# Kernel optimization log

Hardware: AMD Instinct MI355X
Metric: run time of the kernel (lower is better)

## Reference

```python
import jax, jax.numpy as jnp
import numpy as np

N_HEADS = 16
ROPE_BASE = 10000.0

def apply_rope(x):
    # x: [B, H, S, D] with D even; interleaved-pair RoPE (torchtune style)
    B, H, S, D = x.shape
    half = D // 2
    inv_freq = 1.0 / (ROPE_BASE ** (jnp.arange(0, half, dtype=jnp.float32) / half))
    angles = jnp.arange(S, dtype=jnp.float32)[:, None] * inv_freq[None, :]  # [S, D/2]
    cos = jnp.cos(angles)[None, None]  # [1,1,S,D/2]
    sin = jnp.sin(angles)[None, None]
    x1 = x[..., 0::2]
    x2 = x[..., 1::2]
    r1 = x1 * cos - x2 * sin
    r2 = x1 * sin + x2 * cos
    return jnp.stack([r1, r2], axis=-1).reshape(B, H, S, D)

def setup_inputs() -> dict:
    key = jax.random.key(0)
    ks = jax.random.split(key, 5)
    B, S, E = 2, 2048, 1024
    d_attn = 1024
    scale = 1.0 / np.sqrt(E)
    x = jax.random.normal(ks[0], (B, S, E), dtype=jnp.float32)
    Wq = jax.random.normal(ks[1], (d_attn, E), dtype=jnp.float32) * scale
    Wk = jax.random.normal(ks[2], (d_attn, E), dtype=jnp.float32) * scale
    Wv = jax.random.normal(ks[3], (d_attn, E), dtype=jnp.float32) * scale
    Wo = jax.random.normal(ks[4], (E, d_attn), dtype=jnp.float32) * scale
    return {"x": x, "Wq": Wq, "Wk": Wk, "Wv": Wv, "Wo": Wo}

def reference(x, Wq, Wk, Wv, Wo):
    B, S, E = x.shape
    d_attn = Wq.shape[0]
    hd = d_attn // N_HEADS
    attn_scale = 1.0 / np.sqrt(d_attn)
    # projections (nn.Linear: x @ W.T), split heads -> [B, H, S, hd]
    q = (x @ Wq.T).reshape(B, S, N_HEADS, hd).transpose(0, 2, 1, 3)
    k = (x @ Wk.T).reshape(B, S, N_HEADS, hd).transpose(0, 2, 1, 3)
    v = (x @ Wv.T).reshape(B, S, N_HEADS, hd).transpose(0, 2, 1, 3)
    q = apply_rope(q)
    k = apply_rope(k)
    scores = jnp.einsum('bhqd,bhkd->bhqk', q, k) * attn_scale  # [B,H,S,S]
    causal = jnp.tril(jnp.ones((S, S), dtype=bool))
    scores = jnp.where(causal[None, None], scores, -jnp.inf)
    probs = jax.nn.softmax(scores, axis=-1)  # dropout is identity in eval
    out = jnp.einsum('bhqk,bhkd->bhqd', probs, v)
    out = out.transpose(0, 2, 1, 3).reshape(B, S, d_attn)
    return out @ Wo.T
```

## Files before the change

kernel.cpp:

```cpp
#include <hip/hip_runtime.h>


typedef float  f32x4  __attribute__((ext_vector_type(4)));
typedef short  short8 __attribute__((ext_vector_type(8)));

#define MFMA16(a,b,c) __builtin_amdgcn_mfma_f32_16x16x32_bf16((a),(b),(c),0,0,0)
#define GLD_LDS16(g, l)                                                        \
  __builtin_amdgcn_global_load_lds(                                            \
      (const __attribute__((address_space(1))) unsigned int*)(g),              \
      (__attribute__((address_space(3))) unsigned int*)(l), 16, 0, 0)

__device__ __forceinline__ unsigned short f2bf(float f) {
  unsigned int x = __float_as_uint(f);
  x += 0x7fffu + ((x >> 16) & 1u);
  return (unsigned short)(x >> 16);
}
__device__ __forceinline__ float bf2f(unsigned short u) {
  return __uint_as_float(((unsigned int)u) << 16);
}

__global__ __launch_bounds__(256) void cvt_all(const float* __restrict__ x,
                                               const float* __restrict__ wq,
                                               const float* __restrict__ wk,
                                               const float* __restrict__ wv,
                                               const float* __restrict__ wo,
                                               ushort* __restrict__ dst) {
  const int i = blockIdx.x * 256 + threadIdx.x;
  const float* src;
  int off;
  if (i < 1048576) { src = x; off = i; }
  else {
    const int j = i - 1048576;
    const int wsel = j >> 18;
    off = j & 262143;
    src = (wsel == 0) ? wq : (wsel == 1) ? wk : (wsel == 2) ? wv : wo;
  }
  const float4 v = ((const float4*)src)[off];
  ushort4 o = make_ushort4(f2bf(v.x), f2bf(v.y), f2bf(v.z), f2bf(v.w));
  ((ushort4*)dst)[i] = o;
}

template<int MODE, int BN>
__global__ __launch_bounds__(256) void gemm_bt(const ushort* __restrict__ A,
                                               const ushort* __restrict__ B,
                                               void* __restrict__ Cv,
                                               int K) {
  constexpr int NI = BN / 32;
  __shared__ __align__(16) short As[128 * 32];
  __shared__ __align__(16) short Bs[BN * 32];
  const int tid  = threadIdx.x;
  const int lane = tid & 63, w = tid >> 6;
  const int ln   = lane & 15, quad = lane >> 4;
  const int wm   = w >> 1, wn = w & 1;
  const int m0 = blockIdx.y * 128, n0 = blockIdx.x * BN;

  const int srow = lane >> 2;
  const int schk = (lane & 3) * 8;
  const ushort* Ag0 = A + (size_t)(m0 + w * 32      + srow) * K + schk;
  const ushort* Ag1 = A + (size_t)(m0 + w * 32 + 16 + srow) * K + schk;
  const int brow = (BN == 128) ? w * 32 : w * 16;
  const ushort* Bg0 = B + (size_t)(n0 + brow + srow) * K + schk;
  const ushort* Bg1 = B + (size_t)(n0 + brow + 16 + srow) * K + schk;
  short* lA0 = As + (w * 32) * 32;
  short* lA1 = As + (w * 32 + 16) * 32;
  short* lB0 = Bs + brow * 32;
  short* lB1 = Bs + (brow + 16) * 32;

  int aoff[4], boff[NI];
#pragma unroll
  for (int i = 0; i < 4; i++)
    aoff[i] = (wm * 64 + i * 16 + ln) * 32 + quad * 8;
#pragma unroll
  for (int i = 0; i < NI; i++)
    boff[i] = (wn * (BN / 2) + i * 16 + ln) * 32 + quad * 8;
  f32x4 acc[4][NI] = {};

  for (int kt = 0; kt < K; kt += 32) {
    __syncthreads();
    GLD_LDS16(Ag0 + kt, lA0);
    GLD_LDS16(Ag1 + kt, lA1);
    GLD_LDS16(Bg0 + kt, lB0);
    if (BN == 128) GLD_LDS16(Bg1 + kt, lB1);
    __syncthreads();
    short8 av[4], bv[NI];
#pragma unroll
    for (int i = 0; i < 4; i++) av[i] = *(const short8*)&As[aoff[i]];
#pragma unroll
    for (int i = 0; i < NI; i++) bv[i] = *(const short8*)&Bs[boff[i]];
#pragma unroll
    for (int mi = 0; mi < 4; mi++)
#pragma unroll
      for (int ni = 0; ni < NI; ni++)
        acc[mi][ni] = MFMA16(av[mi], bv[ni], acc[mi][ni]);
  }

  if (MODE == 0) {
    ushort* Cq = (ushort*)Cv;
    if (n0 < 2048) {
      ushort* dst = Cq + (n0 < 1024 ? 0 : 4194304);
      const int nbase = (n0 < 1024) ? n0 : n0 - 1024;
#pragma unroll
      for (int mi = 0; mi < 4; mi++) {
        const int row = m0 + wm * 64 + mi * 16 + quad * 4;
#pragma unroll
        for (int ni = 0; ni < NI; ni++) {
          const int col = nbase + wn * (BN / 2) + ni * 16 + ln;
#pragma unroll
          for (int r = 0; r < 4; r++)
            dst[(size_t)(row + r) * 1024 + col] = f2bf(acc[mi][ni][r]);
        }
      }
    } else {
      ushort* vt = Cq + 8388608;
#pragma unroll
      for (int mi = 0; mi < 4; mi++) {
        const int sm = m0 + wm * 64 + mi * 16 + quad * 4;
        const int b = sm >> 11, s = sm & 2047;
#pragma unroll
        for (int ni = 0; ni < NI; ni++) {
          const int nv = (n0 - 2048) + wn * (BN / 2) + ni * 16 + ln;
          const int bh = b * 16 + (nv >> 6), d = nv & 63;
          ushort4 u = make_ushort4(f2bf(acc[mi][ni][0]), f2bf(acc[mi][ni][1]),
                                   f2bf(acc[mi][ni][2]), f2bf(acc[mi][ni][3]));
          *(ushort4*)&vt[((size_t)bh * 64 + d) * 2048 + s] = u;
        }
      }
    }
  } else {
    float* C = (float*)Cv;
#pragma unroll
    for (int mi = 0; mi < 4; mi++) {
      const int row = m0 + wm * 64 + mi * 16 + quad * 4;
#pragma unroll
      for (int ni = 0; ni < NI; ni++) {
        const int col = n0 + wn * (BN / 2) + ni * 16 + ln;
#pragma unroll
        for (int r = 0; r < 4; r++)
          C[(size_t)(row + r) * 1024 + col] = acc[mi][ni][r];
      }
    }
  }
}

__global__ __launch_bounds__(256) void ropek(ushort* __restrict__ qk) {
  const int g  = blockIdx.x * 256 + threadIdx.x;
  const int P0 = g << 2;
  const int mv = P0 >> 9;
  const int s  = mv & 2047;
  const int i0 = P0 & 31;
  const float scale = (mv < 4096) ? 0.04508422002778011f : 1.0f;
  const float sf = (float)s;
  short8 u = *(short8*)&qk[(size_t)P0 * 2];
  short8 ov;
#pragma unroll
  for (int t = 0; t < 4; t++) {
    const float invf = __builtin_amdgcn_exp2f(-(float)(i0 + t) * 0.4152410118579865f);
    const float rev  = sf * invf * 0.15915494309189535f;
    const float rr   = rev - floorf(rev);
    const float sn = __builtin_amdgcn_sinf(rr);
    const float cs = __builtin_amdgcn_cosf(rr);
    const float x1 = bf2f((unsigned short)u[2 * t]);
    const float x2 = bf2f((unsigned short)u[2 * t + 1]);
    ov[2 * t]     = (short)f2bf((x1 * cs - x2 * sn) * scale);
    ov[2 * t + 1] = (short)f2bf((x1 * sn + x2 * cs) * scale);
  }
  *(short8*)&qk[(size_t)P0 * 2] = ov;
}

__global__ __launch_bounds__(256) void attnk(const ushort* __restrict__ q,
                                             const ushort* __restrict__ k,
                                             const ushort* __restrict__ vt,
                                             ushort* __restrict__ Opart,
                                             float* __restrict__ Lpart) {
  __shared__ __align__(16) short Ks[64 * 72];
  __shared__ __align__(16) short Vs[64 * 72];
  __shared__ __align__(16) short Ps[4 * 16 * 72];
  const int tid  = threadIdx.x;
  const int lane = tid & 63, w = tid >> 6;
  const int ln   = lane & 15, quad = lane >> 4;
  const int x = blockIdx.x, bh = blockIdx.y, par = blockIdx.z;
  const int b = bh >> 4, h = bh & 15;
  const int jA = x, jB = 31 - x;
  short* Pw = Ps + w * 1152;

  const size_t qbA = ((size_t)(b * 2048 + jA * 64 + w * 16 + ln)) * 1024 + h * 64;
  const size_t qbB = ((size_t)(b * 2048 + jB * 64 + w * 16 + ln)) * 1024 + h * 64;
  const short8 aqA0 = *(const short8*)&q[qbA + quad * 8];
  const short8 aqA1 = *(const short8*)&q[qbA + 32 + quad * 8];
  const short8 aqB0 = *(const short8*)&q[qbB + quad * 8];
  const short8 aqB1 = *(const short8*)&q[qbB + 32 + quad * 8];

  f32x4 oA[4] = {}, oB[4] = {};
  float lsA[4] = {0.f, 0.f, 0.f, 0.f}, lsB[4] = {0.f, 0.f, 0.f, 0.f};

  const int s0 = tid, s1 = tid + 256;
  const int r0 = s0 >> 3, c0 = (s0 & 7) * 8;
  const int r1 = s1 >> 3, c1 = (s1 & 7) * 8;
  const ushort* kg0 = k  + ((size_t)(b * 2048 + r0)) * 1024 + h * 64 + c0;
  const ushort* kg1 = k  + ((size_t)(b * 2048 + r1)) * 1024 + h * 64 + c1;
  const ushort* vg0 = vt + ((size_t)(bh * 64 + r0)) * 2048 + c0;
  const ushort* vg1 = vt + ((size_t)(bh * 64 + r1)) * 2048 + c1;
  const int wK0 = r0 * 72 + c0, wK1 = r1 * 72 + c1;

  for (int t = par; t <= jB; t += 2) {
    __syncthreads();
    *(short8*)&Ks[wK0] = *(const short8*)(kg0 + (size_t)t * 65536);
    *(short8*)&Ks[wK1] = *(const short8*)(kg1 + (size_t)t * 65536);
    *(short8*)&Vs[wK0] = *(const short8*)(vg0 + t * 64);
    *(short8*)&Vs[wK1] = *(const short8*)(vg1 + t * 64);
    __syncthreads();

    const bool actA = (t <= jA);
    f32x4 scA[4], scB[4];
#pragma unroll
    for (int ct = 0; ct < 4; ct++) {
      const short8 bk0 = *(const short8*)&Ks[(ct * 16 + ln) * 72 + quad * 8];
      const short8 bk1 = *(const short8*)&Ks[(ct * 16 + ln) * 72 + 32 + quad * 8];
      f32x4 z = {0.f, 0.f, 0.f, 0.f};
      z = MFMA16(aqB0, bk0, z);
      z = MFMA16(aqB1, bk1, z);
      scB[ct] = z;
      if (actA) {
        f32x4 y = {0.f, 0.f, 0.f, 0.f};
        y = MFMA16(aqA0, bk0, y);
        y = MFMA16(aqA1, bk1, y);
        scA[ct] = y;
      }
    }
    if (t == jB) {
#pragma unroll
      for (int ct = 0; ct < 4; ct++) {
        const int kv = (t << 6) + ct * 16 + ln;
#pragma unroll
        for (int r = 0; r < 4; r++)
          if (kv > jB * 64 + w * 16 + quad * 4 + r) scB[ct][r] = -100000.0f;
      }
    }
    if (actA && t == jA) {
#pragma unroll
      for (int ct = 0; ct < 4; ct++) {
        const int kv = (t << 6) + ct * 16 + ln;
#pragma unroll
        for (int r = 0; r < 4; r++)
          if (kv > jA * 64 + w * 16 + quad * 4 + r) scA[ct][r] = -100000.0f;
      }
    }

    short8 bv0[4], bv1[4];
#pragma unroll
    for (int dt = 0; dt < 4; dt++) {
      bv0[dt] = *(const short8*)&Vs[(dt * 16 + ln) * 72 + quad * 8];
      bv1[dt] = *(const short8*)&Vs[(dt * 16 + ln) * 72 + 32 + quad * 8];
    }

#pragma unroll
    for (int ct = 0; ct < 4; ct++)
#pragma unroll
      for (int r = 0; r < 4; r++) {
        const float p = __builtin_amdgcn_exp2f(scB[ct][r]);
        lsB[r] += p;
        Pw[(quad * 4 + r) * 72 + ct * 16 + ln] = (short)f2bf(p);
      }
    {
      const short8 ap0 = *(const short8*)&Pw[ln * 72 + quad * 8];
      const short8 ap1 = *(const short8*)&Pw[ln * 72 + 32 + quad * 8];
#pragma unroll
      for (int dt = 0; dt < 4; dt++) {
        oB[dt] = MFMA16(ap0, bv0[dt], oB[dt]);
        oB[dt] = MFMA16(ap1, bv1[dt], oB[dt]);
      }
    }
    if (actA) {
#pragma unroll
      for (int ct = 0; ct < 4; ct++)
#pragma unroll
        for (int r = 0; r < 4; r++) {
          const float p = __builtin_amdgcn_exp2f(scA[ct][r]);
          lsA[r] += p;
          Pw[(quad * 4 + r) * 72 + ct * 16 + ln] = (short)f2bf(p);
        }
      const short8 ap0 = *(const short8*)&Pw[ln * 72 + quad * 8];
      const short8 ap1 = *(const short8*)&Pw[ln * 72 + 32 + quad * 8];
#pragma unroll
      for (int dt = 0; dt < 4; dt++) {
        oA[dt] = MFMA16(ap0, bv0[dt], oA[dt]);
        oA[dt] = MFMA16(ap1, bv1[dt], oA[dt]);
      }
    }
  }

#pragma unroll
  for (int off = 1; off < 16; off <<= 1)
#pragma unroll
    for (int r = 0; r < 4; r++) {
      lsA[r] += __shfl_xor(lsA[r], off, 64);
      lsB[r] += __shfl_xor(lsB[r], off, 64);
    }

  const size_t pidx = ((size_t)(x * 32 + bh)) * 2 + par;
  const size_t ob = pidx * 8192;
#pragma unroll
  for (int r = 0; r < 4; r++) {
    const int row = w * 16 + quad * 4 + r;
#pragma unroll
    for (int dt = 0; dt < 4; dt++) {
      Opart[ob + row * 64 + dt * 16 + ln]        = f2bf(oA[dt][r]);
      Opart[ob + 4096 + row * 64 + dt * 16 + ln] = f2bf(oB[dt][r]);
    }
    if (ln == 0) {
      Lpart[pidx * 128 + row]      = lsA[r];
      Lpart[pidx * 128 + 64 + row] = lsB[r];
    }
  }
}

__global__ __launch_bounds__(256) void mergek(const ushort* __restrict__ Opart,
                                              const float* __restrict__ Lpart,
                                              ushort* __restrict__ ctx) {
  const int x = blockIdx.x, bh = blockIdx.y, tau = blockIdx.z;
  const int b = bh >> 4, h = bh & 15;
  const int j = tau ? 31 - x : x;
  const int tid = threadIdx.x;
  const int row = tid >> 2, c0 = (tid & 3) * 16;
  const size_t p0 = ((size_t)(x * 32 + bh)) * 2;
  const size_t base0 = p0 * 8192 + (size_t)tau * 4096 + row * 64 + c0;
  const size_t base1 = base0 + 8192;
  const float l = Lpart[p0 * 128 + tau * 64 + row] +
                  Lpart[(p0 + 1) * 128 + tau * 64 + row];
  const float inv = 1.0f / l;
  const short8 u0a = *(const short8*)&Opart[base0];
  const short8 u0b = *(const short8*)&Opart[base0 + 8];
  const short8 u1a = *(const short8*)&Opart[base1];
  const short8 u1b = *(const short8*)&Opart[base1 + 8];
  short8 oa, ob;
#pragma unroll
  for (int i = 0; i < 8; i++) {
    oa[i] = (short)f2bf((bf2f((unsigned short)u0a[i]) +
                         bf2f((unsigned short)u1a[i])) * inv);
    ob[i] = (short)f2bf((bf2f((unsigned short)u0b[i]) +
                         bf2f((unsigned short)u1b[i])) * inv);
  }
  const size_t dst = ((size_t)(b * 2048 + j * 64 + row)) * 1024 + h * 64 + c0;
  *(short8*)&ctx[dst]     = oa;
  *(short8*)&ctx[dst + 8] = ob;
}

extern "C" void kernel_launch(void* const* d_in, const int* in_sizes, int n_in,
                              void* d_out, int out_size, void* d_ws, size_t ws_size,
                              hipStream_t stream) {
  const float* x  = (const float*)d_in[0];
  const float* Wq = (const float*)d_in[1];
  const float* Wk = (const float*)d_in[2];
  const float* Wv = (const float*)d_in[3];
  const float* Wo = (const float*)d_in[4];
  float* out = (float*)d_out;
  char* ws = (char*)d_ws;

  ushort* xb  = (ushort*)(ws);
  ushort* wqb = (ushort*)(ws + (size_t)(8  << 20));
  ushort* qb  = (ushort*)(ws + (size_t)(16 << 20));
  ushort* kb  = (ushort*)(ws + (size_t)(24 << 20));
  ushort* vtb = (ushort*)(ws + (size_t)(32 << 20));
  ushort* ctx = (ushort*)(ws + (size_t)(40 << 20));
  float*  lpart = (float*)(ws);
  ushort* opart = (ushort*)d_out;

  cvt_all<<<8192, 256, 0, stream>>>(x, Wq, Wk, Wv, Wo, xb);
  gemm_bt<0, 128><<<dim3(24, 32), 256, 0, stream>>>(xb, wqb, (void*)qb, 1024);
  ropek<<<4096, 256, 0, stream>>>(qb);
  attnk<<<dim3(16, 32, 2), 256, 0, stream>>>(qb, kb, vtb, opart, lpart);
  mergek<<<dim3(16, 32, 2), 256, 0, stream>>>(opart, lpart, ctx);
  gemm_bt<2, 64><<<dim3(16, 32), 256, 0, stream>>>(ctx, wqb + 3145728 , (void*)out, 1024);
}
```

Baseline: 206.2 us.

## Fuse RoPE into QKV GEMM epilogue and drop split-KV attention merge

```diff
diff --git a/kernel.cpp b/kernel.cpp
--- a/kernel.cpp
+++ b/kernel.cpp
@@ -99,6 +99,15 @@
     if (n0 < 2048) {
       ushort* dst = Cq + (n0 < 1024 ? 0 : 4194304);
       const int nbase = (n0 < 1024) ? n0 : n0 - 1024;
+      const float qsc = (n0 < 1024) ? 0.04508422002778011f : 1.0f;
+      const float sgn = (ln & 1) ? 1.0f : -1.0f;
+      float invc[NI];
+#pragma unroll
+      for (int ni = 0; ni < NI; ni++) {
+        const int ii = ni * 8 + (ln >> 1);
+        invc[ni] = __builtin_amdgcn_exp2f(-(float)ii * 0.4152410118579865f) *
+                   0.15915494309189535f;
+      }
 #pragma unroll
       for (int mi = 0; mi < 4; mi++) {
         const int row = m0 + wm * 64 + mi * 16 + quad * 4;
@@ -106,8 +115,17 @@
         for (int ni = 0; ni < NI; ni++) {
           const int col = nbase + wn * (BN / 2) + ni * 16 + ln;
 #pragma unroll
-          for (int r = 0; r < 4; r++)
-            dst[(size_t)(row + r) * 1024 + col] = f2bf(acc[mi][ni][r]);
+          for (int r = 0; r < 4; r++) {
+            const float mine  = acc[mi][ni][r];
+            const float other = __shfl_xor(mine, 1, 64);
+            const int   s     = (row + r) & 2047;
+            const float rev   = (float)s * invc[ni];
+            const float rr    = rev - floorf(rev);
+            const float sn = __builtin_amdgcn_sinf(rr);
+            const float cs = __builtin_amdgcn_cosf(rr);
+            const float rot = (mine * cs + sgn * other * sn) * qsc;
+            dst[(size_t)(row + r) * 1024 + col] = f2bf(rot);
+          }
         }
       }
     } else {
@@ -142,43 +160,17 @@
   }
 }
 
-__global__ __launch_bounds__(256) void ropek(ushort* __restrict__ qk) {
-  const int g  = blockIdx.x * 256 + threadIdx.x;
-  const int P0 = g << 2;
-  const int mv = P0 >> 9;
-  const int s  = mv & 2047;
-  const int i0 = P0 & 31;
-  const float scale = (mv < 4096) ? 0.04508422002778011f : 1.0f;
-  const float sf = (float)s;
-  short8 u = *(short8*)&qk[(size_t)P0 * 2];
-  short8 ov;
-#pragma unroll
-  for (int t = 0; t < 4; t++) {
-    const float invf = __builtin_amdgcn_exp2f(-(float)(i0 + t) * 0.4152410118579865f);
-    const float rev  = sf * invf * 0.15915494309189535f;
-    const float rr   = rev - floorf(rev);
-    const float sn = __builtin_amdgcn_sinf(rr);
-    const float cs = __builtin_amdgcn_cosf(rr);
-    const float x1 = bf2f((unsigned short)u[2 * t]);
-    const float x2 = bf2f((unsigned short)u[2 * t + 1]);
-    ov[2 * t]     = (short)f2bf((x1 * cs - x2 * sn) * scale);
-    ov[2 * t + 1] = (short)f2bf((x1 * sn + x2 * cs) * scale);
-  }
-  *(short8*)&qk[(size_t)P0 * 2] = ov;
-}
-
 __global__ __launch_bounds__(256) void attnk(const ushort* __restrict__ q,
                                              const ushort* __restrict__ k,
                                              const ushort* __restrict__ vt,
-                                             ushort* __restrict__ Opart,
-                                             float* __restrict__ Lpart) {
-  __shared__ __align__(16) short Ks[64 * 72];
-  __shared__ __align__(16) short Vs[64 * 72];
+                                             ushort* __restrict__ ctx) {
+  __shared__ __align__(16) short Ks[128 * 72];
+  __shared__ __align__(16) short Vs[128 * 72];
   __shared__ __align__(16) short Ps[4 * 16 * 72];
   const int tid  = threadIdx.x;
   const int lane = tid & 63, w = tid >> 6;
   const int ln   = lane & 15, quad = lane >> 4;
-  const int x = blockIdx.x, bh = blockIdx.y, par = blockIdx.z;
+  const int x = blockIdx.x, bh = blockIdx.y;
   const int b = bh >> 4, h = bh & 15;
   const int jA = x, jB = 31 - x;
   short* Pw = Ps + w * 1152;
@@ -202,89 +194,102 @@
   const ushort* vg1 = vt + ((size_t)(bh * 64 + r1)) * 2048 + c1;
   const int wK0 = r0 * 72 + c0, wK1 = r1 * 72 + c1;
 
-  for (int t = par; t <= jB; t += 2) {
+  for (int t0 = 0; t0 <= jB; t0 += 2) {
     __syncthreads();
-    *(short8*)&Ks[wK0] = *(const short8*)(kg0 + (size_t)t * 65536);
-    *(short8*)&Ks[wK1] = *(const short8*)(kg1 + (size_t)t * 65536);
-    *(short8*)&Vs[wK0] = *(const short8*)(vg0 + t * 64);
-    *(short8*)&Vs[wK1] = *(const short8*)(vg1 + t * 64);
+    *(short8*)&Ks[wK0] = *(const short8*)(kg0 + (size_t)t0 * 65536);
+    *(short8*)&Ks[wK1] = *(const short8*)(kg1 + (size_t)t0 * 65536);
+    *(short8*)&Vs[wK0] = *(const short8*)(vg0 + t0 * 64);
+    *(short8*)&Vs[wK1] = *(const short8*)(vg1 + t0 * 64);
+    if (t0 + 1 <= jB) {
+      *(short8*)&Ks[4608 + wK0] = *(const short8*)(kg0 + (size_t)(t0 + 1) * 65536);
+      *(short8*)&Ks[4608 + wK1] = *(const short8*)(kg1 + (size_t)(t0 + 1) * 65536);
+      *(short8*)&Vs[4608 + wK0] = *(const short8*)(vg0 + (t0 + 1) * 64);
+      *(short8*)&Vs[4608 + wK1] = *(const short8*)(vg1 + (t0 + 1) * 64);
+    }
     __syncthreads();
 
-    const bool actA = (t <= jA);
-    f32x4 scA[4], scB[4];
-#pragma unroll
-    for (int ct = 0; ct < 4; ct++) {
-      const short8 bk0 = *(const short8*)&Ks[(ct * 16 + ln) * 72 + quad * 8];
-      const short8 bk1 = *(const short8*)&Ks[(ct * 16 + ln) * 72 + 32 + quad * 8];
-      f32x4 z = {0.f, 0.f, 0.f, 0.f};
-      z = MFMA16(aqB0, bk0, z);
-      z = MFMA16(aqB1, bk1, z);
-      scB[ct] = z;
+#pragma unroll
+    for (int u = 0; u < 2; ++u) {
+      const int t = t0 + u;
+      if (t > jB) break;
+      const int koff = u * 4608;
+      const bool actA = (t <= jA);
+
+      f32x4 scA[4], scB[4];
+#pragma unroll
+      for (int ct = 0; ct < 4; ct++) {
+        const short8 bk0 = *(const short8*)&Ks[koff + (ct * 16 + ln) * 72 + quad * 8];
+        const short8 bk1 = *(const short8*)&Ks[koff + (ct * 16 + ln) * 72 + 32 + quad * 8];
+        f32x4 z = {0.f, 0.f, 0.f, 0.f};
+        z = MFMA16(aqB0, bk0, z);
+        z = MFMA16(aqB1, bk1, z);
+        scB[ct] = z;
+        if (actA) {
+          f32x4 y = {0.f, 0.f, 0.f, 0.f};
+          y = MFMA16(aqA0, bk0, y);
+          y = MFMA16(aqA1, bk1, y);
+          scA[ct] = y;
+        }
+      }
+      if (t == jB) {
+#pragma unroll
+        for (int ct = 0; ct < 4; ct++) {
+          const int kv = (t << 6) + ct * 16 + ln;
+#pragma unroll
+          for (int r = 0; r < 4; r++)
+            if (kv > jB * 64 + w * 16 + quad * 4 + r) scB[ct][r] = -100000.0f;
+        }
+      }
+      if (actA && t == jA) {
+#pragma unroll
+        for (int ct = 0; ct < 4; ct++) {
+          const int kv = (t << 6) + ct * 16 + ln;
+#pragma unroll
+          for (int r = 0; r < 4; r++)
+            if (kv > jA * 64 + w * 16 + quad * 4 + r) scA[ct][r] = -100000.0f;
+        }
+      }
+
+      short8 bv0[4], bv1[4];
+#pragma unroll
+      for (int dt = 0; dt < 4; dt++) {
+        bv0[dt] = *(const short8*)&Vs[koff + (dt * 16 + ln) * 72 + quad * 8];
+        bv1[dt] = *(const short8*)&Vs[koff + (dt * 16 + ln) * 72 + 32 + quad * 8];
+      }
+
+#pragma unroll
+      for (int ct = 0; ct < 4; ct++)
+#pragma unroll
+        for (int r = 0; r < 4; r++) {
+          const float p = __builtin_amdgcn_exp2f(scB[ct][r]);
+          lsB[r] += p;
+          Pw[(quad * 4 + r) * 72 + ct * 16 + ln] = (short)f2bf(p);
+        }
+      {
+        const short8 ap0 = *(const short8*)&Pw[ln * 72 + quad * 8];
+        const short8 ap1 = *(const short8*)&Pw[ln * 72 + 32 + quad * 8];
+#pragma unroll
+        for (int dt = 0; dt < 4; dt++) {
+          oB[dt] = MFMA16(ap0, bv0[dt], oB[dt]);
+          oB[dt] = MFMA16(ap1, bv1[dt], oB[dt]);
+        }
+      }
       if (actA) {
-        f32x4 y = {0.f, 0.f, 0.f, 0.f};
-        y = MFMA16(aqA0, bk0, y);
-        y = MFMA16(aqA1, bk1, y);
-        scA[ct] = y;
-      }
-    }
-    if (t == jB) {
-#pragma unroll
-      for (int ct = 0; ct < 4; ct++) {
-        const int kv = (t << 6) + ct * 16 + ln;
-#pragma unroll
-        for (int r = 0; r < 4; r++)
-          if (kv > jB * 64 + w * 16 + quad * 4 + r) scB[ct][r] = -100000.0f;
-      }
-    }
-    if (actA && t == jA) {
-#pragma unroll
-      for (int ct = 0; ct < 4; ct++) {
-        const int kv = (t << 6) + ct * 16 + ln;
-#pragma unroll
-        for (int r = 0; r < 4; r++)
-          if (kv > jA * 64 + w * 16 + quad * 4 + r) scA[ct][r] = -100000.0f;
-      }
-    }
-
-    short8 bv0[4], bv1[4];
-#pragma unroll
-    for (int dt = 0; dt < 4; dt++) {
-      bv0[dt] = *(const short8*)&Vs[(dt * 16 + ln) * 72 + quad * 8];
-      bv1[dt] = *(const short8*)&Vs[(dt * 16 + ln) * 72 + 32 + quad * 8];
-    }
-
-#pragma unroll
-    for (int ct = 0; ct < 4; ct++)
-#pragma unroll
-      for (int r = 0; r < 4; r++) {
-        const float p = __builtin_amdgcn_exp2f(scB[ct][r]);
-        lsB[r] += p;
-        Pw[(quad * 4 + r) * 72 + ct * 16 + ln] = (short)f2bf(p);
-      }
-    {
-      const short8 ap0 = *(const short8*)&Pw[ln * 72 + quad * 8];
-      const short8 ap1 = *(const short8*)&Pw[ln * 72 + 32 + quad * 8];
-#pragma unroll
-      for (int dt = 0; dt < 4; dt++) {
-        oB[dt] = MFMA16(ap0, bv0[dt], oB[dt]);
-        oB[dt] = MFMA16(ap1, bv1[dt], oB[dt]);
-      }
-    }
-    if (actA) {
-#pragma unroll
-      for (int ct = 0; ct < 4; ct++)
-#pragma unroll
-        for (int r = 0; r < 4; r++) {
-          const float p = __builtin_amdgcn_exp2f(scA[ct][r]);
-          lsA[r] += p;
-          Pw[(quad * 4 + r) * 72 + ct * 16 + ln] = (short)f2bf(p);
-        }
-      const short8 ap0 = *(const short8*)&Pw[ln * 72 + quad * 8];
-      const short8 ap1 = *(const short8*)&Pw[ln * 72 + 32 + quad * 8];
-#pragma unroll
-      for (int dt = 0; dt < 4; dt++) {
-        oA[dt] = MFMA16(ap0, bv0[dt], oA[dt]);
-        oA[dt] = MFMA16(ap1, bv1[dt], oA[dt]);
+#pragma unroll
+        for (int ct = 0; ct < 4; ct++)
+#pragma unroll
+          for (int r = 0; r < 4; r++) {
+            const float p = __builtin_amdgcn_exp2f(scA[ct][r]);
+            lsA[r] += p;
+            Pw[(quad * 4 + r) * 72 + ct * 16 + ln] = (short)f2bf(p);
+          }
+        const short8 ap0 = *(const short8*)&Pw[ln * 72 + quad * 8];
+        const short8 ap1 = *(const short8*)&Pw[ln * 72 + 32 + quad * 8];
+#pragma unroll
+        for (int dt = 0; dt < 4; dt++) {
+          oA[dt] = MFMA16(ap0, bv0[dt], oA[dt]);
+          oA[dt] = MFMA16(ap1, bv1[dt], oA[dt]);
+        }
       }
     }
   }
@@ -297,52 +302,20 @@
       lsB[r] += __shfl_xor(lsB[r], off, 64);
     }
 
-  const size_t pidx = ((size_t)(x * 32 + bh)) * 2 + par;
-  const size_t ob = pidx * 8192;
 #pragma unroll
   for (int r = 0; r < 4; r++) {
-    const int row = w * 16 + quad * 4 + r;
+    const float invA = 1.0f / lsA[r];
+    const float invB = 1.0f / lsB[r];
+    const int rowA = jA * 64 + w * 16 + quad * 4 + r;
+    const int rowB = jB * 64 + w * 16 + quad * 4 + r;
 #pragma unroll
     for (int dt = 0; dt < 4; dt++) {
-      Opart[ob + row * 64 + dt * 16 + ln]        = f2bf(oA[dt][r]);
-      Opart[ob + 4096 + row * 64 + dt * 16 + ln] = f2bf(oB[dt][r]);
-    }
-    if (ln == 0) {
-      Lpart[pidx * 128 + row]      = lsA[r];
-      Lpart[pidx * 128 + 64 + row] = lsB[r];
-    }
-  }
-}
-
-__global__ __launch_bounds__(256) void mergek(const ushort* __restrict__ Opart,
-                                              const float* __restrict__ Lpart,
-                                              ushort* __restrict__ ctx) {
-  const int x = blockIdx.x, bh = blockIdx.y, tau = blockIdx.z;
-  const int b = bh >> 4, h = bh & 15;
-  const int j = tau ? 31 - x : x;
-  const int tid = threadIdx.x;
-  const int row = tid >> 2, c0 = (tid & 3) * 16;
-  const size_t p0 = ((size_t)(x * 32 + bh)) * 2;
-  const size_t base0 = p0 * 8192 + (size_t)tau * 4096 + row * 64 + c0;
-  const size_t base1 = base0 + 8192;
-  const float l = Lpart[p0 * 128 + tau * 64 + row] +
-                  Lpart[(p0 + 1) * 128 + tau * 64 + row];
-  const float inv = 1.0f / l;
-  const short8 u0a = *(const short8*)&Opart[base0];
-  const short8 u0b = *(const short8*)&Opart[base0 + 8];
-  const short8 u1a = *(const short8*)&Opart[base1];
-  const short8 u1b = *(const short8*)&Opart[base1 + 8];
-  short8 oa, ob;
-#pragma unroll
-  for (int i = 0; i < 8; i++) {
-    oa[i] = (short)f2bf((bf2f((unsigned short)u0a[i]) +
-                         bf2f((unsigned short)u1a[i])) * inv);
-    ob[i] = (short)f2bf((bf2f((unsigned short)u0b[i]) +
-                         bf2f((unsigned short)u1b[i])) * inv);
-  }
-  const size_t dst = ((size_t)(b * 2048 + j * 64 + row)) * 1024 + h * 64 + c0;
-  *(short8*)&ctx[dst]     = oa;
-  *(short8*)&ctx[dst + 8] = ob;
+      ctx[((size_t)(b * 2048 + rowA)) * 1024 + h * 64 + dt * 16 + ln] =
+          f2bf(oA[dt][r] * invA);
+      ctx[((size_t)(b * 2048 + rowB)) * 1024 + h * 64 + dt * 16 + ln] =
+          f2bf(oB[dt][r] * invB);
+    }
+  }
 }
 
 extern "C" void kernel_launch(void* const* d_in, const int* in_sizes, int n_in,
@@ -362,13 +335,9 @@
   ushort* kb  = (ushort*)(ws + (size_t)(24 << 20));
   ushort* vtb = (ushort*)(ws + (size_t)(32 << 20));
   ushort* ctx = (ushort*)(ws + (size_t)(40 << 20));
-  float*  lpart = (float*)(ws);
-  ushort* opart = (ushort*)d_out;
 
   cvt_all<<<8192, 256, 0, stream>>>(x, Wq, Wk, Wv, Wo, xb);
   gemm_bt<0, 128><<<dim3(24, 32), 256, 0, stream>>>(xb, wqb, (void*)qb, 1024);
-  ropek<<<4096, 256, 0, stream>>>(qb);
-  attnk<<<dim3(16, 32, 2), 256, 0, stream>>>(qb, kb, vtb, opart, lpart);
-  mergek<<<dim3(16, 32, 2), 256, 0, stream>>>(opart, lpart, ctx);
+  attnk<<<dim3(16, 32), 256, 0, stream>>>(qb, kb, vtb, ctx);
   gemm_bt<2, 64><<<dim3(16, 32), 256, 0, stream>>>(ctx, wqb + 3145728 , (void*)out, 1024);
 }
```

Result: slower. 223.8 us (+8.5%).
